# Kernel optimization log

Measured on AMD Instinct MI355X. Metric: run time of the kernel, lower is better.

The kernel has to match this reference:

```python
import jax, jax.numpy as jnp
import numpy as np
from jax import lax

ALPHA = 0.98
DELTA = 2.0
R = 0.5
S = 0.025
EPS = 1e-6


def setup_inputs() -> dict:
    key = jax.random.key(0)
    # non-negative energy spectrogram [B, n_mels, T]
    x = jax.random.uniform(key, (64, 128, 4000), dtype=jnp.float32)
    return {"x": x}


def _pcen(x):
    # x: [B, C, T]; EMA smoother: smooth[0] = x[0], smooth[t] = (1-s)*smooth[t-1] + s*x[t]
    xt = jnp.moveaxis(x, -1, 0)  # [T, B, C]

    def step(carry, x_t):
        sm = (1.0 - S) * carry + S * x_t
        return sm, sm

    init = xt[0]
    _, sm_rest = lax.scan(step, init, xt[1:])  # [T-1, B, C]
    smooth = jnp.concatenate([init[None], sm_rest], axis=0)  # [T, B, C]
    smooth = jnp.moveaxis(smooth, 0, -1)  # [B, C, T]
    pcen = (x / (smooth + EPS) ** ALPHA + DELTA) ** R - DELTA ** R
    return pcen


def reference(x):
    return _pcen(x)
```

## Files before the change

kernel.cpp:

```cpp
#include <hip/hip_runtime.h>
#include <math.h>


constexpr int   TLEN = 4000;
constexpr int   NF4  = 1000;
constexpr int   NTH  = 256;
constexpr float S_C  = 0.025f;
constexpr float A_1  = 1.0f - S_C;

constexpr float fpow(float b, int n) {
    float r = 1.0f;
    for (int i = 0; i < n; ++i) r *= b;
    return r;
}
constexpr float A_2 = fpow(A_1, 2);
constexpr float A_3 = fpow(A_1, 3);
constexpr float A_4 = fpow(A_1, 4);

constexpr float ALPHA = 0.98f;
constexpr float EPS_C = 1e-6f;
constexpr float SQRT2 = 1.41421356237309515f;

__device__ __forceinline__ float pcen_elem(float x, float sm) {
    float t = sm + EPS_C;
    float p = exp2f(-ALPHA * __log2f(t));
    float y = fmaf(x, p, 2.0f);
    return y * __frsqrt_rn(y) - SQRT2;
}

__global__ __launch_bounds__(NTH) void pcen_kernel(const float* __restrict__ x,
                                                   float* __restrict__ out) {
    const int    tid  = threadIdx.x;
    const int    lane = tid & 63;
    const int    wv   = tid >> 6;
    const size_t base = (size_t)blockIdx.x * TLEN;

    const float4* __restrict__ x4 = (const float4*)(x + base);
    float4*       __restrict__ o4 = (float4*)(out + base);

    float4 v[4];
    bool   act[4];
#pragma unroll
    for (int k = 0; k < 4; ++k) {
        int f4 = tid + NTH * k;
        act[k] = (f4 < NF4);
        v[k]   = act[k] ? x4[f4] : make_float4(0.f, 0.f, 0.f, 0.f);
    }

    float A[4], B[4];
#pragma unroll
    for (int k = 0; k < 4; ++k) {
        float4 r  = v[k];
        float  b0 = (tid == 0 && k == 0) ? r.x : S_C * r.x;
        float  w  = fmaf(A_3, b0, S_C * fmaf(A_2, r.y, fmaf(A_1, r.z, r.w)));
        A[k] = act[k] ? A_4 : 1.0f;
        B[k] = act[k] ? w   : 0.0f;
    }

#pragma unroll
    for (int d = 1; d < 64; d <<= 1) {
        float Ap[4], Bp[4];
#pragma unroll
        for (int k = 0; k < 4; ++k) {
            Ap[k] = __shfl_up(A[k], d);
            Bp[k] = __shfl_up(B[k], d);
        }
        if (lane >= d) {
#pragma unroll
            for (int k = 0; k < 4; ++k) {
                B[k] = fmaf(A[k], Bp[k], B[k]);
                A[k] = A[k] * Ap[k];
            }
        }
    }

    __shared__ float sA[4][4], sB[4][4];
    if (lane == 63) {
#pragma unroll
        for (int k = 0; k < 4; ++k) { sA[k][wv] = A[k]; sB[k][wv] = B[k]; }
    }
    __syncthreads();

    float E[4];
#pragma unroll
    for (int k = 0; k < 4; ++k) {
        int   lim = 4 * k + wv;
        float e   = 0.0f;
        for (int m = 0; m < 15; ++m) {
            if (m < lim) e = fmaf(sA[m >> 2][m & 3], e, sB[m >> 2][m & 3]);
        }
        E[k] = e;
    }

#pragma unroll
    for (int k = 0; k < 4; ++k) {
        float Ai = __shfl_up(A[k], 1);
        float Bi = __shfl_up(B[k], 1);
        if (lane == 0) { Ai = 1.0f; Bi = 0.0f; }
        float sm = fmaf(Ai, E[k], Bi);

        float4 r  = v[k];
        float  b0 = (tid == 0 && k == 0) ? r.x : S_C * r.x;
        float  s0 = fmaf(A_1, sm, b0);
        float  s1 = fmaf(A_1, s0, S_C * r.y);
        float  s2 = fmaf(A_1, s1, S_C * r.z);
        float  s3 = fmaf(A_1, s2, S_C * r.w);

        float4 o;
        o.x = pcen_elem(r.x, s0);
        o.y = pcen_elem(r.y, s1);
        o.z = pcen_elem(r.z, s2);
        o.w = pcen_elem(r.w, s3);

        int f4 = tid + NTH * k;
        if (act[k]) o4[f4] = o;
    }
}

extern "C" void kernel_launch(void* const* d_in, const int* in_sizes, int n_in,
                              void* d_out, int out_size, void* d_ws, size_t ws_size,
                              hipStream_t stream) {
    const float* x   = (const float*)d_in[0];
    float*       out = (float*)d_out;
    const int nch    = in_sizes[0] / TLEN;
    pcen_kernel<<<nch, NTH, 0, stream>>>(x, out);
}
```

Measured before the change: 227.6 us.

## Exploit constant decay factor in scan and use raw AMDGPU math intrinsics

The per-element multiplier in the linear recurrence is the constant (1-s)^4, so the wave-level scan now carries only the B term. It multiplies by compile-time powers of (1-s) instead of shuffling and combining A values, which halves the shuffle traffic. The cross-wave combine uses the constant (1-s)^256 and straight-line per-wave chains. The per-lane prefix factor is computed with a single exp2. pcen_elem switches to the raw hardware exp2, log and sqrt builtins, trading some accuracy and denormal handling for fewer instructions.

New measurement: 226.0 us. About the same (-0.7%).

```diff
diff --git a/kernel.cpp b/kernel.cpp
--- a/kernel.cpp
+++ b/kernel.cpp
@@ -13,9 +13,11 @@
     for (int i = 0; i < n; ++i) r *= b;
     return r;
 }
-constexpr float A_2 = fpow(A_1, 2);
-constexpr float A_3 = fpow(A_1, 3);
-constexpr float A_4 = fpow(A_1, 4);
+constexpr float A_2  = fpow(A_1, 2);
+constexpr float A_3  = fpow(A_1, 3);
+constexpr float A256 = fpow(A_1, 256);
+
+constexpr float L2A4 = -0.14610359f;
 
 constexpr float ALPHA = 0.98f;
 constexpr float EPS_C = 1e-6f;
@@ -23,9 +25,9 @@
 
 __device__ __forceinline__ float pcen_elem(float x, float sm) {
     float t = sm + EPS_C;
-    float p = exp2f(-ALPHA * __log2f(t));
+    float p = __builtin_amdgcn_exp2f(-ALPHA * __builtin_amdgcn_logf(t));
     float y = fmaf(x, p, 2.0f);
-    return y * __frsqrt_rn(y) - SQRT2;
+    return __builtin_amdgcn_sqrtf(y) - SQRT2;
 }
 
 __global__ __launch_bounds__(NTH) void pcen_kernel(const float* __restrict__ x,
@@ -47,57 +49,71 @@
         v[k]   = act[k] ? x4[f4] : make_float4(0.f, 0.f, 0.f, 0.f);
     }
 
-    float A[4], B[4];
+    float B[4];
 #pragma unroll
     for (int k = 0; k < 4; ++k) {
         float4 r  = v[k];
         float  b0 = (tid == 0 && k == 0) ? r.x : S_C * r.x;
-        float  w  = fmaf(A_3, b0, S_C * fmaf(A_2, r.y, fmaf(A_1, r.z, r.w)));
-        A[k] = act[k] ? A_4 : 1.0f;
-        B[k] = act[k] ? w   : 0.0f;
+        B[k] = fmaf(A_3, b0, S_C * fmaf(A_2, r.y, fmaf(A_1, r.z, r.w)));
     }
 
+    constexpr float CD[6] = { fpow(A_1, 4),  fpow(A_1, 8),   fpow(A_1, 16),
+                              fpow(A_1, 32), fpow(A_1, 64),  fpow(A_1, 128) };
 #pragma unroll
-    for (int d = 1; d < 64; d <<= 1) {
-        float Ap[4], Bp[4];
+    for (int s = 0; s < 6; ++s) {
+        const int   d = 1 << s;
+        const float c = CD[s];
+        float Bp[4];
 #pragma unroll
-        for (int k = 0; k < 4; ++k) {
-            Ap[k] = __shfl_up(A[k], d);
-            Bp[k] = __shfl_up(B[k], d);
-        }
-        if (lane >= d) {
+        for (int k = 0; k < 4; ++k) Bp[k] = __shfl_up(B[k], d);
+        const bool ok = (lane >= d);
 #pragma unroll
-            for (int k = 0; k < 4; ++k) {
-                B[k] = fmaf(A[k], Bp[k], B[k]);
-                A[k] = A[k] * Ap[k];
-            }
-        }
+        for (int k = 0; k < 4; ++k) B[k] = fmaf(c, ok ? Bp[k] : 0.0f, B[k]);
     }
 
-    __shared__ float sA[4][4], sB[4][4];
+    __shared__ float sB[16];
     if (lane == 63) {
 #pragma unroll
-        for (int k = 0; k < 4; ++k) { sA[k][wv] = A[k]; sB[k][wv] = B[k]; }
+        for (int k = 0; k < 4; ++k) sB[4 * k + wv] = B[k];
     }
     __syncthreads();
 
-    float E[4];
-#pragma unroll
-    for (int k = 0; k < 4; ++k) {
-        int   lim = 4 * k + wv;
-        float e   = 0.0f;
-        for (int m = 0; m < 15; ++m) {
-            if (m < lim) e = fmaf(sA[m >> 2][m & 3], e, sB[m >> 2][m & 3]);
+    float E0, E1, E2, E3;
+    {
+        float e = 0.0f;
+#define CH(m) e = fmaf(A256, e, sB[m]);
+        if (wv == 0) {
+            E0 = e;
+            CH(0) CH(1) CH(2)  E1 = fmaf(A256, e, sB[3]);  CH(3)
+            CH(4) CH(5) CH(6)  E2 = fmaf(A256, e, sB[7]);  CH(7)
+            CH(8) CH(9) CH(10) E3 = fmaf(A256, e, sB[11]);
+        } else if (wv == 1) {
+            CH(0)  E0 = e;
+            CH(1) CH(2) CH(3)  CH(4)  E1 = e;
+            CH(5) CH(6) CH(7)  CH(8)  E2 = e;
+            CH(9) CH(10) CH(11) CH(12) E3 = e;
+        } else if (wv == 2) {
+            CH(0) CH(1)  E0 = e;
+            CH(2) CH(3) CH(4) CH(5)   E1 = e;
+            CH(6) CH(7) CH(8) CH(9)   E2 = e;
+            CH(10) CH(11) CH(12) CH(13) E3 = e;
+        } else {
+            CH(0) CH(1) CH(2)  E0 = e;
+            CH(3) CH(4) CH(5) CH(6)   E1 = e;
+            CH(7) CH(8) CH(9) CH(10)  E2 = e;
+            CH(11) CH(12) CH(13) CH(14) E3 = e;
         }
-        E[k] = e;
+#undef CH
     }
+    const float E[4] = { E0, E1, E2, E3 };
+
+    const float Al = __builtin_amdgcn_exp2f((float)lane * L2A4);
 
 #pragma unroll
     for (int k = 0; k < 4; ++k) {
-        float Ai = __shfl_up(A[k], 1);
         float Bi = __shfl_up(B[k], 1);
-        if (lane == 0) { Ai = 1.0f; Bi = 0.0f; }
-        float sm = fmaf(Ai, E[k], Bi);
+        if (lane == 0) Bi = 0.0f;
+        float sm = fmaf(Al, E[k], Bi);
 
         float4 r  = v[k];
         float  b0 = (tid == 0 && k == 0) ? r.x : S_C * r.x;
```
